# Optimization experiments

Hardware: AMD Instinct MI355X
Metric: run time of the kernel (lower is better)

## Reference

```python
import jax, jax.numpy as jnp
import numpy as np

N_NODES = 50000
N_EDGES = 800000
IN_CH = 128
OUT_CH = 64
HEADS = 4
NEG_SLOPE = 0.2  # PyG GATConv default


def setup_inputs() -> dict:
    key = jax.random.key(0)
    k1, k2, k3, k4, k5 = jax.random.split(key, 5)
    x = jax.random.normal(k1, (N_NODES, IN_CH), dtype=jnp.float32)
    edge_index = jax.random.randint(k2, (2, N_EDGES), 0, N_NODES, dtype=jnp.int64)
    W = jax.random.normal(k3, (HEADS * OUT_CH, IN_CH), dtype=jnp.float32) * (1.0 / np.sqrt(IN_CH))
    att_src = jax.random.normal(k4, (HEADS, OUT_CH), dtype=jnp.float32) * (1.0 / np.sqrt(OUT_CH))
    att_dst = jax.random.normal(k5, (HEADS, OUT_CH), dtype=jnp.float32) * (1.0 / np.sqrt(OUT_CH))
    bias = jnp.zeros((OUT_CH,), dtype=jnp.float32)
    return {"x": x, "edge_index": edge_index, "W": W,
            "att_src": att_src, "att_dst": att_dst, "bias": bias}


def reference(x, edge_index, W, att_src, att_dst, bias):
    # GAT2NO_NORM.forward in eval mode: dropout == identity.
    N = x.shape[0]
    H, C = att_src.shape
    # PyG GATConv adds self-loops by default.
    loop = jnp.arange(N, dtype=edge_index.dtype)
    src = jnp.concatenate([edge_index[0], loop])  # message source j
    dst = jnp.concatenate([edge_index[1], loop])  # message target i
    # Linear projection, reshape to heads: [N, H, C]
    h = (x @ W.T).reshape(N, H, C)
    # Per-node attention halves: [N, H]
    a_src = jnp.einsum('nhc,hc->nh', h, att_src)
    a_dst = jnp.einsum('nhc,hc->nh', h, att_dst)
    # Per-edge raw score, LeakyReLU: [E, H]
    e = jax.nn.leaky_relu(a_src[src] + a_dst[dst], NEG_SLOPE)
    # Segment (edge-)softmax over incoming edges of each dst node.
    m = jax.lax.stop_gradient(jax.ops.segment_max(e, dst, num_segments=N))
    ex = jnp.exp(e - m[dst])
    denom = jax.ops.segment_sum(ex, dst, num_segments=N)
    alpha = ex / denom[dst]  # self-loops guarantee denom > 0
    # Weighted scatter-sum of messages: [N, H, C]
    msg = h[src] * alpha[:, :, None]
    out = jax.ops.segment_sum(msg, dst, num_segments=N)
    # concat=False -> mean over heads, then bias, then ReLU (module wrapper)
    out = out.mean(axis=1) + bias
    return jax.nn.relu(out)
```

## Files before the change

### kernel.cpp

```cpp
#include <hip/hip_runtime.h>
#include <hip/hip_fp16.h>
#include <math.h>

#define N_NODES 50000
#define N_EDGES 800000
#define IN_CH 128
#define PROJ_CH 256
#define OUT_CH 64
#define HEADS 4
#define NEG_SLOPE 0.2f
#define CAP 80
#define PROJ_BLOCKS 782
#define GRID_BLOCKS 3125

typedef _Float16 f16x8 __attribute__((ext_vector_type(8)));
typedef _Float16 f16x4 __attribute__((ext_vector_type(4)));
typedef __fp16   hf2   __attribute__((ext_vector_type(2)));
typedef float    f32x4 __attribute__((ext_vector_type(4)));

__device__ __forceinline__ float leaky(float v) {
    return v > 0.f ? v : NEG_SLOPE * v;
}

__device__ __forceinline__ hf2 u32_as_h2(unsigned int u) {
    union { unsigned int u; hf2 h; } c; c.u = u; return c.h;
}

__global__ __launch_bounds__(256) void mega_kernel(
    const float* __restrict__ x, const float* __restrict__ W,
    const float* __restrict__ att_src, const float* __restrict__ att_dst,
    const int* __restrict__ ei, int* __restrict__ cnt, unsigned short* __restrict__ csr,
    _Float16* __restrict__ h, float* __restrict__ a_src, float* __restrict__ a_dst)
{
    __shared__ _Float16 xs[64 * 136];
    const int tid = threadIdx.x;
    const int bid = blockIdx.x;

    const int e = bid * 256 + tid;
    const int esrc = ei[e];
    const int edst = ei[N_EDGES + e];

    if (bid >= PROJ_BLOCKS) {
        int pos = atomicAdd(&cnt[edst], 1);
        if (pos < CAP) csr[edst * CAP + pos] = (unsigned short)esrc;
        return;
    }

    const int w    = tid >> 6;
    const int lane = tid & 63;
    const int q    = lane >> 4;
    const int l15  = lane & 15;
    const int nb   = bid * 64;

    f16x8 B[4][4];
#pragma unroll
    for (int k0i = 0; k0i < 4; ++k0i)
#pragma unroll
        for (int n0i = 0; n0i < 4; ++n0i) {
            const int oc = w * 64 + n0i * 16 + l15;
            const float* src = W + (size_t)oc * IN_CH + k0i * 32 + q * 8;
            float4 s0 = *(const float4*)src;
            float4 s1 = *(const float4*)(src + 4);
            f16x8 v;
            v[0] = (_Float16)s0.x; v[1] = (_Float16)s0.y;
            v[2] = (_Float16)s0.z; v[3] = (_Float16)s0.w;
            v[4] = (_Float16)s1.x; v[5] = (_Float16)s1.y;
            v[6] = (_Float16)s1.z; v[7] = (_Float16)s1.w;
            B[k0i][n0i] = v;
        }

#pragma unroll
    for (int r = 0; r < 8; ++r) {
        int v   = r * 256 + tid;
        int row = v >> 5;
        int c4  = v & 31;
        int grow = nb + row;
        if (grow > N_NODES - 1) grow = N_NODES - 1;
        float4 xv = *(const float4*)(x + (size_t)grow * IN_CH + c4 * 4);
        f16x4 hv;
        hv[0] = (_Float16)xv.x; hv[1] = (_Float16)xv.y;
        hv[2] = (_Float16)xv.z; hv[3] = (_Float16)xv.w;
        *(f16x4*)&xs[row * 136 + c4 * 4] = hv;
    }
    __syncthreads();

    const int pos = atomicAdd(&cnt[edst], 1);

    f32x4 acc[4][4];
#pragma unroll
    for (int m0i = 0; m0i < 4; ++m0i)
#pragma unroll
        for (int n0i = 0; n0i < 4; ++n0i)
            acc[m0i][n0i] = (f32x4){0.f, 0.f, 0.f, 0.f};

#pragma unroll
    for (int k0i = 0; k0i < 4; ++k0i) {
        f16x8 A[4];
#pragma unroll
        for (int m0i = 0; m0i < 4; ++m0i)
            A[m0i] = *(const f16x8*)&xs[(m0i * 16 + l15) * 136 + k0i * 32 + q * 8];
#pragma unroll
        for (int n0i = 0; n0i < 4; ++n0i)
#pragma unroll
            for (int m0i = 0; m0i < 4; ++m0i)
                acc[m0i][n0i] = __builtin_amdgcn_mfma_f32_16x16x32_f16(
                    A[m0i], B[k0i][n0i], acc[m0i][n0i], 0, 0, 0);
    }

    float att_s[4], att_d[4];
#pragma unroll
    for (int n0i = 0; n0i < 4; ++n0i) {
        att_s[n0i] = att_src[w * 64 + n0i * 16 + l15];
        att_d[n0i] = att_dst[w * 64 + n0i * 16 + l15];
    }

#pragma unroll
    for (int m0i = 0; m0i < 4; ++m0i) {
        float vs[4], vd[4];
#pragma unroll
        for (int r = 0; r < 4; ++r) {
            float s = 0.f, d = 0.f;
#pragma unroll
            for (int n0i = 0; n0i < 4; ++n0i) {
                s = fmaf(acc[m0i][n0i][r], att_s[n0i], s);
                d = fmaf(acc[m0i][n0i][r], att_d[n0i], d);
            }
            vs[r] = s; vd[r] = d;
        }
#pragma unroll
        for (int off = 1; off < 16; off <<= 1) {
#pragma unroll
            for (int r = 0; r < 4; ++r) {
                vs[r] += __shfl_xor(vs[r], off, 64);
                vd[r] += __shfl_xor(vd[r], off, 64);
            }
        }
#pragma unroll
        for (int r = 0; r < 4; ++r) {
            int node = nb + m0i * 16 + q * 4 + r;
            if (l15 == 0 && node < N_NODES) {
                a_src[node * HEADS + w] = vs[r];
                a_dst[node * HEADS + w] = vd[r];
            }
        }
#pragma unroll
        for (int r = 0; r < 4; ++r) {
            int node = nb + m0i * 16 + q * 4 + r;
            if (node < N_NODES) {
#pragma unroll
                for (int n0i = 0; n0i < 4; ++n0i)
                    h[(size_t)node * PROJ_CH + w * 64 + n0i * 16 + l15] =
                        (_Float16)acc[m0i][n0i][r];
            }
        }
    }

    if (pos < CAP) csr[edst * CAP + pos] = (unsigned short)esrc;
}

__global__ __launch_bounds__(256) void aggregate_kernel(
    const _Float16* __restrict__ h, const float* __restrict__ a_src,
    const float* __restrict__ a_dst, const int* __restrict__ cnt,
    const unsigned short* __restrict__ csr, const float* __restrict__ bias,
    float* __restrict__ out)
{
    const int tid  = threadIdx.x;
    const int wave = tid >> 6;
    const int l    = tid & 63;
    const int i    = blockIdx.x * 4 + wave;

    __shared__ float lw_all[4][(CAP + 1) * 4];
    __shared__ int   lj_all[4][CAP + 4];
    float* lw = lw_all[wave];
    int*   lj = lj_all[wave];

    const int n    = min(cnt[i], CAP);
    const int base = i * CAP;
    const int h4   = l & 3;
    const float adh = a_dst[i * 4 + h4];

    float lsum = 0.f;
    {
        float ws = __expf(leaky(a_src[i * 4 + h4] + adh));
        if (l < 4) { lw[l] = ws; lsum = ws; }
        if (l == 0) lj[0] = i;
    }

    const int erel = l >> 2;
    for (int p0 = 0; p0 < n; p0 += 16) {
        int e = p0 + erel;
        bool valid = e < n;
        int j = valid ? (int)csr[base + e] : 0;
        float w = 0.f;
        if (valid) w = __expf(leaky(a_src[j * 4 + h4] + adh));
        lsum += w;
        lw[(e + 1) * 4 + h4] = w;
        if (h4 == 0) lj[e + 1] = j;
    }
#pragma unroll
    for (int off = 4; off < 64; off <<= 1) lsum += __shfl_xor(lsum, off, 64);

    __syncthreads();

    const int half_ = l >> 5;
    const int jj    = l & 31;
    const int hd    = jj >> 3;
    const int m_total = n + 1;
    const uint4* hv = (const uint4*)h;

    float acc[8];
#pragma unroll
    for (int k = 0; k < 8; ++k) acc[k] = 0.f;

    for (int qq = 0; qq < m_total; qq += 8) {
        const int eb = qq + 4 * half_;
        int ia[4]; float wa[4];
#pragma unroll
        for (int k = 0; k < 4; ++k) {
            int e = eb + k;
            ia[k] = (e < m_total) ? e : 0;
            wa[k] = (e < m_total) ? lw[ia[k] * 4 + hd] : 0.f;
        }
        uint4 d0 = hv[(size_t)lj[ia[0]] * 32 + jj];
        uint4 d1 = hv[(size_t)lj[ia[1]] * 32 + jj];
        uint4 d2 = hv[(size_t)lj[ia[2]] * 32 + jj];
        uint4 d3 = hv[(size_t)lj[ia[3]] * 32 + jj];
        hf2 wab = __builtin_amdgcn_cvt_pkrtz(wa[0], wa[1]);
        hf2 wcd = __builtin_amdgcn_cvt_pkrtz(wa[2], wa[3]);

        const unsigned int* A0 = (const unsigned int*)&d0;
        const unsigned int* A1 = (const unsigned int*)&d1;
        const unsigned int* A2 = (const unsigned int*)&d2;
        const unsigned int* A3 = (const unsigned int*)&d3;
#pragma unroll
        for (int k = 0; k < 4; ++k) {
            unsigned int lo01 = __builtin_amdgcn_perm(A1[k], A0[k], 0x05040100u);
            unsigned int hi01 = __builtin_amdgcn_perm(A1[k], A0[k], 0x07060302u);
            acc[2 * k]     = __builtin_amdgcn_fdot2(u32_as_h2(lo01), wab, acc[2 * k], false);
            acc[2 * k + 1] = __builtin_amdgcn_fdot2(u32_as_h2(hi01), wab, acc[2 * k + 1], false);
            unsigned int lo23 = __builtin_amdgcn_perm(A3[k], A2[k], 0x05040100u);
            unsigned int hi23 = __builtin_amdgcn_perm(A3[k], A2[k], 0x07060302u);
            acc[2 * k]     = __builtin_amdgcn_fdot2(u32_as_h2(lo23), wcd, acc[2 * k], false);
            acc[2 * k + 1] = __builtin_amdgcn_fdot2(u32_as_h2(hi23), wcd, acc[2 * k + 1], false);
        }
    }

#pragma unroll
    for (int k = 0; k < 8; ++k) acc[k] += __shfl_xor(acc[k], 32, 64);

    float linv = 1.f / __shfl(lsum, hd, 64);
#pragma unroll
    for (int k = 0; k < 8; ++k) {
        float r = acc[k] * linv;
        r += __shfl_xor(r, 8, 64);
        r += __shfl_xor(r, 16, 64);
        acc[k] = r;
    }

    if (l < 8) {
        float* op = out + (size_t)i * OUT_CH + l * 8;
        float4 o0, o1;
        o0.x = fmaxf(0.25f * acc[0] + bias[l * 8 + 0], 0.f);
        o0.y = fmaxf(0.25f * acc[1] + bias[l * 8 + 1], 0.f);
        o0.z = fmaxf(0.25f * acc[2] + bias[l * 8 + 2], 0.f);
        o0.w = fmaxf(0.25f * acc[3] + bias[l * 8 + 3], 0.f);
        o1.x = fmaxf(0.25f * acc[4] + bias[l * 8 + 4], 0.f);
        o1.y = fmaxf(0.25f * acc[5] + bias[l * 8 + 5], 0.f);
        o1.z = fmaxf(0.25f * acc[6] + bias[l * 8 + 6], 0.f);
        o1.w = fmaxf(0.25f * acc[7] + bias[l * 8 + 7], 0.f);
        *(float4*)op = o0;
        *((float4*)op + 1) = o1;
    }
}

extern "C" void kernel_launch(void* const* d_in, const int* in_sizes, int n_in,
                              void* d_out, int out_size, void* d_ws, size_t ws_size,
                              hipStream_t stream)
{
    const float* x       = (const float*)d_in[0];
    const int*   ei      = (const int*)d_in[1];
    const float* W       = (const float*)d_in[2];
    const float* att_src = (const float*)d_in[3];
    const float* att_dst = (const float*)d_in[4];
    const float* bias    = (const float*)d_in[5];
    float* out = (float*)d_out;

    _Float16* h   = (_Float16*)d_ws;
    float* asrc  = (float*)(h + (size_t)N_NODES * PROJ_CH);
    float* adst  = asrc + (size_t)N_NODES * HEADS;
    int*   cnt   = (int*)(adst + (size_t)N_NODES * HEADS);
    unsigned short* csr = (unsigned short*)(cnt + N_NODES);

    (void)hipMemsetAsync(cnt, 0, N_NODES * sizeof(int), stream);
    hipLaunchKernelGGL(mega_kernel, dim3(GRID_BLOCKS), dim3(256), 0, stream,
                       x, W, att_src, att_dst, ei, cnt, csr, h, asrc, adst);
    hipLaunchKernelGGL(aggregate_kernel, dim3(N_NODES / 4), dim3(256), 0, stream,
                       h, asrc, adst, cnt, csr, bias, out);
}
```

Before: 196.0 us.

## Fuse memset, projection, CSR build and aggregation into one cooperative persistent kernel

Replaces the memset plus two-kernel launch sequence with a single cooperative persistent kernel. Grid-wide syncs separate three phases: zeroing counts, GEMM projection with CSR scatter, and per-node aggregation. This removes launch gaps and the separate memset. In exchange it adds grid-sync costs and limits parallelism to resident blocks, so phases now run as strided loops rather than oversubscribed grids. It falls back to the old path if the cooperative launch fails.

Result: slower. 434.1 us (+121.5%).

```diff
diff --git a/kernel.cpp b/kernel.cpp
--- a/kernel.cpp
+++ b/kernel.cpp
@@ -1,6 +1,9 @@
 #include <hip/hip_runtime.h>
 #include <hip/hip_fp16.h>
+#include <hip/hip_cooperative_groups.h>
 #include <math.h>
+
+namespace cg = cooperative_groups;
 
 #define N_NODES 50000
 #define N_EDGES 800000
@@ -12,6 +15,7 @@
 #define CAP 80
 #define PROJ_BLOCKS 782
 #define GRID_BLOCKS 3125
+#define AGG_GROUPS 12500
 
 typedef _Float16 f16x8 __attribute__((ext_vector_type(8)));
 typedef _Float16 f16x4 __attribute__((ext_vector_type(4)));
@@ -26,31 +30,17 @@
     union { unsigned int u; hf2 h; } c; c.u = u; return c.h;
 }
 
-__global__ __launch_bounds__(256) void mega_kernel(
+__device__ __forceinline__ void gemm_tile(
+    int nb, int tid,
     const float* __restrict__ x, const float* __restrict__ W,
     const float* __restrict__ att_src, const float* __restrict__ att_dst,
-    const int* __restrict__ ei, int* __restrict__ cnt, unsigned short* __restrict__ csr,
-    _Float16* __restrict__ h, float* __restrict__ a_src, float* __restrict__ a_dst)
-{
-    __shared__ _Float16 xs[64 * 136];
-    const int tid = threadIdx.x;
-    const int bid = blockIdx.x;
-
-    const int e = bid * 256 + tid;
-    const int esrc = ei[e];
-    const int edst = ei[N_EDGES + e];
-
-    if (bid >= PROJ_BLOCKS) {
-        int pos = atomicAdd(&cnt[edst], 1);
-        if (pos < CAP) csr[edst * CAP + pos] = (unsigned short)esrc;
-        return;
-    }
-
+    _Float16* __restrict__ h, float* __restrict__ a_src, float* __restrict__ a_dst,
+    _Float16* xs)
+{
     const int w    = tid >> 6;
     const int lane = tid & 63;
     const int q    = lane >> 4;
     const int l15  = lane & 15;
-    const int nb   = bid * 64;
 
     f16x8 B[4][4];
 #pragma unroll
@@ -84,8 +74,6 @@
     }
     __syncthreads();
 
-    const int pos = atomicAdd(&cnt[edst], 1);
-
     f32x4 acc[4][4];
 #pragma unroll
     for (int m0i = 0; m0i < 4; ++m0i)
@@ -154,26 +142,15 @@
             }
         }
     }
-
-    if (pos < CAP) csr[edst * CAP + pos] = (unsigned short)esrc;
-}
-
-__global__ __launch_bounds__(256) void aggregate_kernel(
+}
+
+__device__ __forceinline__ void aggregate_node(
+    int i, int l,
     const _Float16* __restrict__ h, const float* __restrict__ a_src,
     const float* __restrict__ a_dst, const int* __restrict__ cnt,
     const unsigned short* __restrict__ csr, const float* __restrict__ bias,
-    float* __restrict__ out)
-{
-    const int tid  = threadIdx.x;
-    const int wave = tid >> 6;
-    const int l    = tid & 63;
-    const int i    = blockIdx.x * 4 + wave;
-
-    __shared__ float lw_all[4][(CAP + 1) * 4];
-    __shared__ int   lj_all[4][CAP + 4];
-    float* lw = lw_all[wave];
-    int*   lj = lj_all[wave];
-
+    float* __restrict__ out, float* lw, int* lj)
+{
     const int n    = min(cnt[i], CAP);
     const int base = i * CAP;
     const int h4   = l & 3;
@@ -273,6 +250,92 @@
     }
 }
 
+__global__ __launch_bounds__(256) void fused_kernel(
+    const float* __restrict__ x, const float* __restrict__ W,
+    const float* __restrict__ att_src, const float* __restrict__ att_dst,
+    const int* __restrict__ ei, const float* __restrict__ bias,
+    float* __restrict__ out, int* __restrict__ cnt,
+    unsigned short* __restrict__ csr, _Float16* __restrict__ h,
+    float* __restrict__ a_src, float* __restrict__ a_dst)
+{
+    cg::grid_group gg = cg::this_grid();
+
+    __shared__ _Float16 xs[64 * 136];
+    __shared__ float lw_all[4][(CAP + 1) * 4];
+    __shared__ int   lj_all[4][CAP + 4];
+
+    const int tid = threadIdx.x;
+    const int bid = blockIdx.x;
+    const int G   = gridDim.x;
+
+    for (int t = bid * 256 + tid; t < N_NODES; t += G * 256) cnt[t] = 0;
+    gg.sync();
+
+    for (int tb = bid; tb < PROJ_BLOCKS; tb += G) {
+        gemm_tile(tb * 64, tid, x, W, att_src, att_dst, h, a_src, a_dst, xs);
+        __syncthreads();
+    }
+    for (int e = bid * 256 + tid; e < N_EDGES; e += G * 256) {
+        int esrc = ei[e];
+        int edst = ei[N_EDGES + e];
+        int pos = atomicAdd(&cnt[edst], 1);
+        if (pos < CAP) csr[edst * CAP + pos] = (unsigned short)esrc;
+    }
+
+    __threadfence();
+    gg.sync();
+    __threadfence();
+
+    const int wave = tid >> 6;
+    const int l    = tid & 63;
+    for (int ib = bid; ib < AGG_GROUPS; ib += G) {
+        aggregate_node(ib * 4 + wave, l, h, a_src, a_dst, cnt, csr, bias, out,
+                       lw_all[wave], lj_all[wave]);
+        __syncthreads();
+    }
+}
+
+__global__ __launch_bounds__(256) void mega_kernel(
+    const float* __restrict__ x, const float* __restrict__ W,
+    const float* __restrict__ att_src, const float* __restrict__ att_dst,
+    const int* __restrict__ ei, int* __restrict__ cnt, unsigned short* __restrict__ csr,
+    _Float16* __restrict__ h, float* __restrict__ a_src, float* __restrict__ a_dst)
+{
+    __shared__ _Float16 xs[64 * 136];
+    const int tid = threadIdx.x;
+    const int bid = blockIdx.x;
+
+    const int e = bid * 256 + tid;
+    const int esrc = ei[e];
+    const int edst = ei[N_EDGES + e];
+
+    if (bid >= PROJ_BLOCKS) {
+        int pos = atomicAdd(&cnt[edst], 1);
+        if (pos < CAP) csr[edst * CAP + pos] = (unsigned short)esrc;
+        return;
+    }
+
+    gemm_tile(bid * 64, tid, x, W, att_src, att_dst, h, a_src, a_dst, xs);
+
+    int pos = atomicAdd(&cnt[edst], 1);
+    if (pos < CAP) csr[edst * CAP + pos] = (unsigned short)esrc;
+}
+
+__global__ __launch_bounds__(256) void aggregate_kernel(
+    const _Float16* __restrict__ h, const float* __restrict__ a_src,
+    const float* __restrict__ a_dst, const int* __restrict__ cnt,
+    const unsigned short* __restrict__ csr, const float* __restrict__ bias,
+    float* __restrict__ out)
+{
+    __shared__ float lw_all[4][(CAP + 1) * 4];
+    __shared__ int   lj_all[4][CAP + 4];
+    const int tid  = threadIdx.x;
+    const int wave = tid >> 6;
+    const int l    = tid & 63;
+    aggregate_node(blockIdx.x * 4 + wave, l, h, a_src, a_dst, cnt, csr, bias, out,
+                   lw_all[wave], lj_all[wave]);
+}
+
 extern "C" void kernel_launch(void* const* d_in, const int* in_sizes, int n_in,
                               void* d_out, int out_size, void* d_ws, size_t ws_size,
                               hipStream_t stream)
@@ -291,9 +354,28 @@
     int*   cnt   = (int*)(adst + (size_t)N_NODES * HEADS);
     unsigned short* csr = (unsigned short*)(cnt + N_NODES);
 
-    (void)hipMemsetAsync(cnt, 0, N_NODES * sizeof(int), stream);
-    hipLaunchKernelGGL(mega_kernel, dim3(GRID_BLOCKS), dim3(256), 0, stream,
-                       x, W, att_src, att_dst, ei, cnt, csr, h, asrc, adst);
-    hipLaunchKernelGGL(aggregate_kernel, dim3(N_NODES / 4), dim3(256), 0, stream,
-                       h, asrc, adst, cnt, csr, bias, out);
-}
+    bool ok = false;
+    int nbpc = 0;
+    hipError_t oe = hipOccupancyMaxActiveBlocksPerMultiprocessor(
+        &nbpc, fused_kernel, 256, 0);
+    if (oe == hipSuccess && nbpc > 0) {
+        int grid = nbpc * 256;
+        if (grid > GRID_BLOCKS) grid = GRID_BLOCKS;
+        void* args[] = {
+            (void*)&x, (void*)&W, (void*)&att_src, (void*)&att_dst,
+            (void*)&ei, (void*)&bias, (void*)&out,
+            (void*)&cnt, (void*)&csr, (void*)&h, (void*)&asrc, (void*)&adst
+        };
+        hipError_t le = hipLaunchCooperativeKernel(
+            (const void*)fused_kernel, dim3(grid), dim3(256), args, 0, stream);
+        ok = (le == hipSuccess);
+    }
+
+    if (!ok) {
+        (void)hipMemsetAsync(cnt, 0, N_NODES * sizeof(int), stream);
+        hipLaunchKernelGGL(mega_kernel, dim3(GRID_BLOCKS), dim3(256), 0, stream,
+                           x, W, att_src, att_dst, ei, cnt, csr, h, asrc, adst);
+        hipLaunchKernelGGL(aggregate_kernel, dim3(AGG_GROUPS), dim3(256), 0, stream,
+                           h, asrc, adst, cnt, csr, bias, out);
+    }
+}
```

## Interleave projection and CSR-fill blocks, stage h stores through LDS

Applied to the files above, without the earlier changes.

Even blocks now do the projection and odd blocks build the CSR, so the two kinds of work mix across the GPU. Each fill block handles 1024 edges with batched loads and atomics, which replaces the old scheme of one edge per thread over 3125 blocks. The projection output is written to a wider LDS tile first and then stored to h as coalesced 16-byte rows, instead of scattered 2-byte stores. The cost is an extra LDS round-trip with two syncs, and fewer fill blocks, each doing more serial atomic work.

Measured after the change: 198.2 us. No clear change (+1.1%).

```diff
diff --git a/kernel.cpp b/kernel.cpp
--- a/kernel.cpp
+++ b/kernel.cpp
@@ -11,7 +11,10 @@
 #define NEG_SLOPE 0.2f
 #define CAP 80
 #define PROJ_BLOCKS 782
-#define GRID_BLOCKS 3125
+#define FILL_BLOCKS 782
+#define MEGA_BLOCKS (PROJ_BLOCKS + FILL_BLOCKS)
+#define AGG_GROUPS 12500
+#define LDSW 264
 
 typedef _Float16 f16x8 __attribute__((ext_vector_type(8)));
 typedef _Float16 f16x4 __attribute__((ext_vector_type(4)));
@@ -32,25 +35,36 @@
     const int* __restrict__ ei, int* __restrict__ cnt, unsigned short* __restrict__ csr,
     _Float16* __restrict__ h, float* __restrict__ a_src, float* __restrict__ a_dst)
 {
-    __shared__ _Float16 xs[64 * 136];
+    __shared__ _Float16 xs[64 * LDSW];
     const int tid = threadIdx.x;
     const int bid = blockIdx.x;
 
-    const int e = bid * 256 + tid;
-    const int esrc = ei[e];
-    const int edst = ei[N_EDGES + e];
-
-    if (bid >= PROJ_BLOCKS) {
-        int pos = atomicAdd(&cnt[edst], 1);
-        if (pos < CAP) csr[edst * CAP + pos] = (unsigned short)esrc;
+    if (bid & 1) {
+        const int fb = bid >> 1;
+        const int base = fb * 1024;
+        int es[4], ed[4], ps[4];
+#pragma unroll
+        for (int k = 0; k < 4; ++k) {
+            int e = base + k * 256 + tid;
+            if (e < N_EDGES) { es[k] = ei[e]; ed[k] = ei[N_EDGES + e]; }
+            else ed[k] = -1;
+        }
+#pragma unroll
+        for (int k = 0; k < 4; ++k)
+            if (ed[k] >= 0) ps[k] = atomicAdd(&cnt[ed[k]], 1);
+#pragma unroll
+        for (int k = 0; k < 4; ++k)
+            if (ed[k] >= 0 && ps[k] < CAP)
+                csr[ed[k] * CAP + ps[k]] = (unsigned short)es[k];
         return;
     }
 
+    const int gb   = bid >> 1;
     const int w    = tid >> 6;
     const int lane = tid & 63;
     const int q    = lane >> 4;
     const int l15  = lane & 15;
-    const int nb   = bid * 64;
+    const int nb   = gb * 64;
 
     f16x8 B[4][4];
 #pragma unroll
@@ -84,8 +98,6 @@
     }
     __syncthreads();
 
-    const int pos = atomicAdd(&cnt[edst], 1);
-
     f32x4 acc[4][4];
 #pragma unroll
     for (int m0i = 0; m0i < 4; ++m0i)
@@ -143,19 +155,31 @@
                 a_dst[node * HEADS + w] = vd[r];
             }
         }
+    }
+
+    __syncthreads();
+#pragma unroll
+    for (int m0i = 0; m0i < 4; ++m0i)
 #pragma unroll
         for (int r = 0; r < 4; ++r) {
-            int node = nb + m0i * 16 + q * 4 + r;
-            if (node < N_NODES) {
-#pragma unroll
-                for (int n0i = 0; n0i < 4; ++n0i)
-                    h[(size_t)node * PROJ_CH + w * 64 + n0i * 16 + l15] =
-                        (_Float16)acc[m0i][n0i][r];
-            }
-        }
-    }
-
-    if (pos < CAP) csr[edst * CAP + pos] = (unsigned short)esrc;
+            int row = m0i * 16 + q * 4 + r;
+#pragma unroll
+            for (int n0i = 0; n0i < 4; ++n0i)
+                xs[row * LDSW + w * 64 + n0i * 16 + l15] =
+                    (_Float16)acc[m0i][n0i][r];
+        }
+    __syncthreads();
+
+#pragma unroll
+    for (int s = 0; s < 8; ++s) {
+        int row = s * 8 + (tid >> 5);
+        int col = (tid & 31) * 8;
+        int node = nb + row;
+        if (node < N_NODES) {
+            f16x8 v = *(const f16x8*)&xs[row * LDSW + col];
+            *(f16x8*)(h + (size_t)node * PROJ_CH + col) = v;
+        }
+    }
 }
 
 __global__ __launch_bounds__(256) void aggregate_kernel(
@@ -292,8 +316,8 @@
     unsigned short* csr = (unsigned short*)(cnt + N_NODES);
 
     (void)hipMemsetAsync(cnt, 0, N_NODES * sizeof(int), stream);
-    hipLaunchKernelGGL(mega_kernel, dim3(GRID_BLOCKS), dim3(256), 0, stream,
+    hipLaunchKernelGGL(mega_kernel, dim3(MEGA_BLOCKS), dim3(256), 0, stream,
                        x, W, att_src, att_dst, ei, cnt, csr, h, asrc, adst);
-    hipLaunchKernelGGL(aggregate_kernel, dim3(N_NODES / 4), dim3(256), 0, stream,
+    hipLaunchKernelGGL(aggregate_kernel, dim3(AGG_GROUPS), dim3(256), 0, stream,
                        h, asrc, adst, cnt, csr, bias, out);
 }
```
